# Kernel tuning notes

Hardware: AMD Instinct MI355X
Metric: run time of the kernel (lower is better)

The kernel has to match this reference:

```python
import jax, jax.numpy as jnp
import numpy as np

EMBED_DIM = 1024
Q_HEADS = 8
KV_HEADS = 4
HEAD_DIM = EMBED_DIM // Q_HEADS          # 128
KV_EMBED_DIM = HEAD_DIM * KV_HEADS       # 512
LN_EPS = 1e-5
RMS_EPS = 1e-6


def _activation_quant(x):
    # per-token int8 quant over last dim
    scale = 127.0 / jnp.clip(jnp.max(jnp.abs(x), axis=-1, keepdims=True), 1e-5)
    return jnp.clip(jnp.round(x * scale), -128, 127) / scale


def _weight_quant(w):
    # ternary (sign) quant with global mean-abs scale
    scale = jnp.mean(jnp.abs(w))
    e = jnp.mean(w)
    return jnp.sign(w - e) * scale


def bit_linear(x, w):
    # fresh RMSNorm with weight=ones (as in the torch code: RMSNorm(d)(x))
    x_norm = x * jax.lax.rsqrt(jnp.mean(x * x, axis=-1, keepdims=True) + RMS_EPS)
    # straight-through estimators
    x_q = x_norm + jax.lax.stop_gradient(_activation_quant(x_norm) - x_norm)
    w_q = w + jax.lax.stop_gradient(_weight_quant(w) - w)
    # F.linear(x_quant, w_quant): NO bias (the torch forward ignores self.bias)
    return jnp.einsum('bnd,od->bno', x_q, w_q)


def setup_inputs() -> dict:
    key = jax.random.key(0)
    ks = jax.random.split(key, 7)
    B, S = 4, 2048

    def xavier(k, shape):
        std = (2.0 / (shape[0] + shape[1])) ** 0.5
        return std * jax.random.normal(k, shape, dtype=jnp.float32)

    return {
        'query': jax.random.normal(ks[0], (B, S, EMBED_DIM), dtype=jnp.float32),
        'key':   jax.random.normal(ks[1], (B, S, EMBED_DIM), dtype=jnp.float32),
        'value': jax.random.normal(ks[2], (B, S, EMBED_DIM), dtype=jnp.float32),
        'q_w':   xavier(ks[3], (EMBED_DIM, EMBED_DIM)),
        'k_w':   xavier(ks[4], (KV_EMBED_DIM, EMBED_DIM)),
        'v_w':   xavier(ks[5], (KV_EMBED_DIM, EMBED_DIM)),
        'out_w': xavier(ks[6], (EMBED_DIM, KV_EMBED_DIM)),
        'ln_gamma': jnp.ones((KV_EMBED_DIM,), dtype=jnp.float32),
        'ln_beta':  jnp.zeros((KV_EMBED_DIM,), dtype=jnp.float32),
    }


def reference(query, key, value, q_w, k_w, v_w, out_w, ln_gamma, ln_beta):
    B, N, _ = query.shape
    q = bit_linear(query, q_w)   # [b, n, embed_dim]
    k = bit_linear(key,   k_w)   # [b, s, kv_embed_dim]
    v = bit_linear(value, v_w)   # [b, s, kv_embed_dim]

    g = Q_HEADS // KV_HEADS  # head groups
    # b n (hq d) -> b hq n d -> b hk g n d  (head index = h*g + g_idx, matching
    # einops 'b (h g) n d -> b g h n d')
    q = q.reshape(B, N, Q_HEADS, HEAD_DIM).transpose(0, 2, 1, 3)
    q = q.reshape(B, KV_HEADS, g, N, HEAD_DIM)
    k = k.reshape(B, -1, KV_HEADS, HEAD_DIM).transpose(0, 2, 1, 3)  # b h s d
    v = v.reshape(B, -1, KV_HEADS, HEAD_DIM).transpose(0, 2, 1, 3)  # b h s d

    scale = HEAD_DIM ** 0.5
    q = q / scale
    # note: the original SUMS over the group axis g (faithful to einops einsum)
    sim = jnp.einsum('bhgnd,bhsd->bhns', q, k)
    # note: original divides by scale AGAIN before softmax
    attn = jax.nn.softmax(sim / scale, axis=-1)
    out = jnp.einsum('bhns,bhsd->bnhd', attn, v)        # b n hk d
    x = out.reshape(B, N, KV_EMBED_DIM)

    # LayerNorm over kv_embed_dim
    mu = jnp.mean(x, axis=-1, keepdims=True)
    var = jnp.mean((x - mu) ** 2, axis=-1, keepdims=True)
    x = (x - mu) * jax.lax.rsqrt(var + LN_EPS) * ln_gamma + ln_beta

    return bit_linear(x, out_w)  # [b, n, embed_dim]
```

## Files before the change

kernel.cpp:

```cpp
#include <hip/hip_runtime.h>
#include <cstdint>
#include <cstddef>

constexpr int B_   = 4;
constexpr int SEQ  = 2048;
constexpr int E    = 1024;
constexpr int KVE  = 512;
constexpr int H    = 4;
constexpr int ROWS = B_ * SEQ;

typedef short short8   __attribute__((ext_vector_type(8)));
typedef short short4v  __attribute__((ext_vector_type(4)));
typedef float floatx4  __attribute__((ext_vector_type(4)));
typedef float floatx16 __attribute__((ext_vector_type(16)));
typedef int   intx4    __attribute__((ext_vector_type(4)));

__device__ inline short f2bf(float f) {
    uint32_t u = __builtin_bit_cast(uint32_t, f);
    u = (u + 0x7fff + ((u >> 16) & 1)) >> 16;
    return (short)u;
}
__device__ inline float bf2f(short s) {
    return __builtin_bit_cast(float, (uint32_t)(uint16_t)s << 16);
}
__device__ inline void gl_lds16(const void* g, void* l) {
    __builtin_amdgcn_global_load_lds(
        (const __attribute__((address_space(1))) unsigned int*)g,
        (__attribute__((address_space(3))) unsigned int*)l, 16, 0, 0);
}

__global__ __launch_bounds__(256) void pre_kernel(
    const float* __restrict__ qx, const float* __restrict__ kx,
    const float* __restrict__ vx,
    const float* __restrict__ w0, const float* __restrict__ w1,
    const float* __restrict__ w2, const float* __restrict__ w3,
    int8_t* __restrict__ xq01, int8_t* __restrict__ xq2,
    float* __restrict__ dqv, float* __restrict__ stats)
{
    int tid = threadIdx.x, bid = blockIdx.x;
    int lane = tid & 63, wv = tid >> 6;
    if (bid < 256) {
        int m = bid >> 6;
        const float* w = (m == 0) ? w0 : (m == 1) ? w1 : (m == 2) ? w2 : w3;
        int n4 = ((m == 0) ? 1024 * 1024 : 512 * 1024) >> 2;
        float s = 0.f, sa = 0.f;
        for (int i = (bid & 63) * 256 + tid; i < n4; i += 64 * 256) {
            float4 x = ((const float4*)w)[i];
            s += x.x + x.y + x.z + x.w;
            sa += fabsf(x.x) + fabsf(x.y) + fabsf(x.z) + fabsf(x.w);
        }
#pragma unroll
        for (int o = 32; o; o >>= 1) { s += __shfl_xor(s, o); sa += __shfl_xor(sa, o); }
        __shared__ float ls[4], lsa[4];
        if (!lane) { ls[wv] = s; lsa[wv] = sa; }
        __syncthreads();
        if (!tid) {
            atomicAdd(&stats[2 * m],     ls[0] + ls[1] + ls[2] + ls[3]);
            atomicAdd(&stats[2 * m + 1], lsa[0] + lsa[1] + lsa[2] + lsa[3]);
        }
        return;
    }
    int rowi = (bid - 256) * 4 + wv;
    int z = rowi >> 13, r = rowi & (ROWS - 1);
    const float* x = (z == 0) ? qx : (z == 1) ? kx : vx;
    int8_t* xq = (z == 2) ? xq2 : xq01 + (size_t)z * ROWS * E;
    size_t base = (size_t)r * E;
    float4 v[4];
    float ss = 0.f, am = 0.f;
#pragma unroll
    for (int j = 0; j < 4; j++) {
        v[j] = *(const float4*)(x + base + lane * 4 + j * 256);
        ss += v[j].x * v[j].x + v[j].y * v[j].y + v[j].z * v[j].z + v[j].w * v[j].w;
        am = fmaxf(am, fmaxf(fmaxf(fabsf(v[j].x), fabsf(v[j].y)),
                             fmaxf(fabsf(v[j].z), fabsf(v[j].w))));
    }
#pragma unroll
    for (int o = 32; o; o >>= 1) { ss += __shfl_xor(ss, o); am = fmaxf(am, __shfl_xor(am, o)); }
    float rms = rsqrtf(ss * (1.0f / E) + 1e-6f);
    float cl  = fmaxf(am * rms, 1e-5f);
    float kf  = rms * (127.0f / cl);
#pragma unroll
    for (int j = 0; j < 4; j++) {
        int q0 = max(-128, min(127, (int)rintf(v[j].x * kf)));
        int q1 = max(-128, min(127, (int)rintf(v[j].y * kf)));
        int q2 = max(-128, min(127, (int)rintf(v[j].z * kf)));
        int q3 = max(-128, min(127, (int)rintf(v[j].w * kf)));
        uint32_t pk = (uint32_t)(q0 & 0xff) | ((uint32_t)(q1 & 0xff) << 8) |
                      ((uint32_t)(q2 & 0xff) << 16) | ((uint32_t)(q3 & 0xff) << 24);
        *(uint32_t*)(xq + base + lane * 4 + j * 256) = pk;
    }
    if (!lane) dqv[(size_t)z * ROWS + r] = cl * (1.0f / 127.0f);
}

__global__ __launch_bounds__(256) void wquant_kernel(
    const float* __restrict__ w0, const float* __restrict__ w1,
    const float* __restrict__ w2, const float* __restrict__ w3,
    int n0, int n1, int n2, int n3, const float* __restrict__ stats,
    int8_t* __restrict__ o0, int8_t* __restrict__ o1,
    int8_t* __restrict__ o2, int8_t* __restrict__ o3)
{
    int m = blockIdx.y;
    const float* w = (m == 0) ? w0 : (m == 1) ? w1 : (m == 2) ? w2 : w3;
    int n = (m == 0) ? n0 : (m == 1) ? n1 : (m == 2) ? n2 : n3;
    int8_t* o = (m == 0) ? o0 : (m == 1) ? o1 : (m == 2) ? o2 : o3;
    float e = stats[2 * m] / (float)n;
    int n4 = n >> 2;
    for (int i = blockIdx.x * 256 + threadIdx.x; i < n4; i += gridDim.x * 256) {
        float4 x = ((const float4*)w)[i];
        int q0 = (x.x > e) - (x.x < e);
        int q1 = (x.y > e) - (x.y < e);
        int q2 = (x.z > e) - (x.z < e);
        int q3 = (x.w > e) - (x.w < e);
        uint32_t pk = (uint32_t)(q0 & 0xff) | ((uint32_t)(q1 & 0xff) << 8) |
                      ((uint32_t)(q2 & 0xff) << 16) | ((uint32_t)(q3 & 0xff) << 24);
        *(uint32_t*)(o + ((size_t)i << 2)) = pk;
    }
}

template <bool F32OUT>
__device__ inline void gemm_body(
    const int8_t* __restrict__ A, const int8_t* __restrict__ W,
    const float* __restrict__ dqv, float sw, void* __restrict__ Cout,
    int O, int K, int8_t* As, int8_t* Ws, size_t row0, size_t c0)
{
    int tid = threadIdx.x;
    int w = tid >> 6, lane = tid & 63;
    int quad = lane >> 4, l15 = lane & 15;
    int mbase = (w & 1) * 64, nbase = (w >> 1) * 64;

    intx4 acc[4][4];
#pragma unroll
    for (int i = 0; i < 4; i++)
#pragma unroll
        for (int j = 0; j < 4; j++) acc[i][j] = (intx4){0, 0, 0, 0};

    const int8_t* Ag[4]; const int8_t* Wg[4]; int8_t* lA[4]; int8_t* lW[4];
#pragma unroll
    for (int t = 0; t < 4; t++) {
        int c = tid + t * 256;
        int row = c >> 3, g = (c & 7) ^ (row & 7);
        Ag[t] = A + (row0 + row) * K + g * 16;
        Wg[t] = W + (c0 + row) * K + g * 16;
        lA[t] = As + c * 16;
        lW[t] = Ws + c * 16;
    }

    for (int kt = 0; kt < K; kt += 128) {
        __syncthreads();
#pragma unroll
        for (int t = 0; t < 4; t++) {
            gl_lds16(Ag[t] + kt, lA[t]);
            gl_lds16(Wg[t] + kt, lW[t]);
        }
        __syncthreads();
#pragma unroll
        for (int kh = 0; kh < 2; kh++) {
            intx4 af[4], bfr[4];
#pragma unroll
            for (int mt = 0; mt < 4; mt++) {
                int row = mbase + mt * 16 + l15;
                int pos = (quad + 4 * kh) ^ (row & 7);
                af[mt] = *(const intx4*)(As + row * 128 + pos * 16);
            }
#pragma unroll
            for (int nt = 0; nt < 4; nt++) {
                int row = nbase + nt * 16 + l15;
                int pos = (quad + 4 * kh) ^ (row & 7);
                bfr[nt] = *(const intx4*)(Ws + row * 128 + pos * 16);
            }
#pragma unroll
            for (int mt = 0; mt < 4; mt++)
#pragma unroll
                for (int nt = 0; nt < 4; nt++)
                    acc[mt][nt] = __builtin_amdgcn_mfma_i32_16x16x64_i8(
                        af[mt], bfr[nt], acc[mt][nt], 0, 0, 0);
        }
    }

#pragma unroll
    for (int mt = 0; mt < 4; mt++) {
#pragma unroll
        for (int r = 0; r < 4; r++) {
            size_t grow = row0 + mbase + mt * 16 + quad * 4 + r;
            float scv = sw * dqv[grow];
#pragma unroll
            for (int nt = 0; nt < 4; nt++) {
                size_t gcol = c0 + nbase + nt * 16 + l15;
                float v = (float)acc[mt][nt][r] * scv;
                if constexpr (F32OUT) ((float*)Cout)[grow * O + gcol] = v;
                else                  ((short*)Cout)[grow * O + gcol] = f2bf(v);
            }
        }
    }
}

__global__ __launch_bounds__(256) void gemm_qkv(
    const int8_t* __restrict__ xq01, const int8_t* __restrict__ xq2,
    const int8_t* __restrict__ wq_q, const int8_t* __restrict__ wq_k,
    const int8_t* __restrict__ wq_v, const float* __restrict__ dqv,
    const float* __restrict__ stats,
    short* __restrict__ qb, short* __restrict__ kb, short* __restrict__ vb)
{
    __shared__ int8_t As[128 * 128];
    __shared__ int8_t Ws[128 * 128];
    int id = blockIdx.x;
    int z, bx, by;
    if (id < 512)      { z = 0; bx = id & 7; by = id >> 3; }
    else if (id < 768) { z = 1; int t = id - 512; bx = t & 3; by = t >> 2; }
    else               { z = 2; int t = id - 768; bx = t & 3; by = t >> 2; }
    int O = z ? KVE : E;
    const int8_t* A = (z == 0) ? xq01 : (z == 1) ? xq01 + (size_t)ROWS * E : xq2;
    const int8_t* W = (z == 0) ? wq_q : (z == 1) ? wq_k : wq_v;
    short* outp = (z == 0) ? qb : (z == 1) ? kb : vb;
    float sw = stats[2 * z + 1] / (float)(O * E);
    gemm_body<false>(A, W, dqv + (size_t)z * ROWS, sw, outp, O, E, As, Ws,
                     (size_t)by * 128, (size_t)bx * 128);
}

__global__ __launch_bounds__(256) void gemm_out(
    const int8_t* __restrict__ A, const int8_t* __restrict__ W,
    const float* __restrict__ dqv, const float* __restrict__ stats,
    float* __restrict__ Cout)
{
    __shared__ int8_t As[128 * 128];
    __shared__ int8_t Ws[128 * 128];
    float sw = stats[7] / (float)(E * KVE);
    gemm_body<true>(A, W, dqv, sw, Cout, E, KVE, As, Ws,
                    (size_t)blockIdx.y * 128, (size_t)blockIdx.x * 128);
}

__global__ __launch_bounds__(256, 2) void attn_mfma(
    const short* __restrict__ qb, const short* __restrict__ kb,
    const short* __restrict__ vb, short* __restrict__ opart,
    float* __restrict__ mlbuf)
{
    __shared__ short Ks[64][132];
    __shared__ short Vt[128][68];
    __shared__ short Ps[128][68];
    int tid = threadIdx.x;
    int w = tid >> 6, lane = tid & 63;
    int l31 = lane & 31, hi = lane >> 5;
    int blk = blockIdx.x, h = blockIdx.y, half = blockIdx.z;
    int b = blk >> 4;
    size_t qrow0 = (size_t)blk * 128;
    size_t sbase = (size_t)b * SEQ + (size_t)half * (SEQ / 2);

    int sK = tid >> 2, cK = tid & 3;
    int sV = (tid & 15) * 4, dV = tid >> 4;

    short8 kreg[4], vreg[4];
    {
        const short* ksrc = kb + (sbase + sK) * KVE + h * 128 + cK * 32;
#pragma unroll
        for (int j = 0; j < 4; j++) kreg[j] = *(const short8*)(ksrc + j * 8);
        const short* vsrc = vb + (sbase + sV) * KVE + h * 128 + dV * 8;
#pragma unroll
        for (int j = 0; j < 4; j++) vreg[j] = *(const short8*)(vsrc + j * KVE);
    }

    short8 qfrag[8];
    {
        const short* src = qb + (qrow0 + w * 32 + l31) * E + h * 256 + hi * 8;
#pragma unroll
        for (int j = 0; j < 8; j++) {
            short8 a  = *(const short8*)(src + j * 16);
            short8 b2 = *(const short8*)(src + j * 16 + 128);
            short8 o;
#pragma unroll
            for (int e = 0; e < 8; e++)
                o[e] = f2bf((bf2f(a[e]) + bf2f(b2[e])) * (1.0f / 128.0f));
            qfrag[j] = o;
        }
    }

    floatx16 oacc[4];
#pragma unroll
    for (int dt = 0; dt < 4; dt++)
#pragma unroll
        for (int r = 0; r < 16; r++) oacc[dt][r] = 0.f;
    float m_s = -1e30f, l_s = 0.f;

    for (int st = 0; st < SEQ / 128; st++) {
        __syncthreads();
#pragma unroll
        for (int j = 0; j < 4; j++)
            *(short8*)&Ks[sK][cK * 32 + j * 8] = kreg[j];
#pragma unroll
        for (int i = 0; i < 8; i++) {
            short4v vv = { vreg[0][i], vreg[1][i], vreg[2][i], vreg[3][i] };
            *(short4v*)&Vt[dV * 8 + i][sV] = vv;
        }
        if (st + 1 < SEQ / 128) {
            size_t srow0 = sbase + (size_t)(st + 1) * 64;
            const short* ksrc = kb + (srow0 + sK) * KVE + h * 128 + cK * 32;
#pragma unroll
            for (int j = 0; j < 4; j++) kreg[j] = *(const short8*)(ksrc + j * 8);
            const short* vsrc = vb + (srow0 + sV) * KVE + h * 128 + dV * 8;
#pragma unroll
            for (int j = 0; j < 4; j++) vreg[j] = *(const short8*)(vsrc + j * KVE);
        }
        __syncthreads();
        floatx16 sc0, sc1;
#pragma unroll
        for (int r = 0; r < 16; r++) { sc0[r] = 0.f; sc1[r] = 0.f; }
#pragma unroll
        for (int j = 0; j < 8; j++) {
            short8 kf0 = *(const short8*)&Ks[l31][j * 16 + hi * 8];
            short8 kf1 = *(const short8*)&Ks[32 + l31][j * 16 + hi * 8];
            sc0 = __builtin_amdgcn_mfma_f32_32x32x16_bf16(kf0, qfrag[j], sc0, 0, 0, 0);
            sc1 = __builtin_amdgcn_mfma_f32_32x32x16_bf16(kf1, qfrag[j], sc1, 0, 0, 0);
        }
        float mx = sc0[0];
#pragma unroll
        for (int r = 0; r < 16; r++) { mx = fmaxf(mx, sc0[r]); mx = fmaxf(mx, sc1[r]); }
        mx = fmaxf(mx, __shfl_xor(mx, 32));
        float nm = fmaxf(m_s, mx);
        float alpha = __expf(m_s - nm);
        m_s = nm;
        float rs = 0.f;
#pragma unroll
        for (int r = 0; r < 16; r++) {
            float p0 = __expf(sc0[r] - nm); sc0[r] = p0; rs += p0;
            float p1 = __expf(sc1[r] - nm); sc1[r] = p1; rs += p1;
        }
        rs += __shfl_xor(rs, 32);
        l_s = l_s * alpha + rs;
        int qrow = w * 32 + l31;
#pragma unroll
        for (int c = 0; c < 4; c++) {
            short4v p0 = { f2bf(sc0[c * 4]), f2bf(sc0[c * 4 + 1]),
                           f2bf(sc0[c * 4 + 2]), f2bf(sc0[c * 4 + 3]) };
            *(short4v*)&Ps[qrow][c * 8 + hi * 4] = p0;
            short4v p1 = { f2bf(sc1[c * 4]), f2bf(sc1[c * 4 + 1]),
                           f2bf(sc1[c * 4 + 2]), f2bf(sc1[c * 4 + 3]) };
            *(short4v*)&Ps[qrow][32 + c * 8 + hi * 4] = p1;
        }
#pragma unroll
        for (int dt = 0; dt < 4; dt++)
#pragma unroll
            for (int r = 0; r < 16; r++) oacc[dt][r] *= alpha;
        short8 pb[4];
#pragma unroll
        for (int j = 0; j < 4; j++)
            pb[j] = *(const short8*)&Ps[qrow][j * 16 + hi * 8];
#pragma unroll
        for (int dt = 0; dt < 4; dt++)
#pragma unroll
            for (int j = 0; j < 4; j++) {
                short8 vf = *(const short8*)&Vt[dt * 32 + l31][j * 16 + hi * 8];
                oacc[dt] = __builtin_amdgcn_mfma_f32_32x32x16_bf16(vf, pb[j], oacc[dt], 0, 0, 0);
            }
    }
    {
        float inv = 1.0f / l_s;
        size_t grow = qrow0 + w * 32 + l31;
        short* dst = opart + ((size_t)half * ROWS + grow) * KVE + h * 128;
#pragma unroll
        for (int dt = 0; dt < 4; dt++)
#pragma unroll
            for (int c = 0; c < 4; c++) {
                short4v o4 = { f2bf(oacc[dt][c * 4] * inv),
                               f2bf(oacc[dt][c * 4 + 1] * inv),
                               f2bf(oacc[dt][c * 4 + 2] * inv),
                               f2bf(oacc[dt][c * 4 + 3] * inv) };
                *(short4v*)(dst + dt * 32 + c * 8 + hi * 4) = o4;
            }
        if (hi == 0) {
            float* ml = mlbuf + (((size_t)half * ROWS + grow) * H + h) * 2;
            ml[0] = m_s;
            ml[1] = l_s;
        }
    }
}

__global__ __launch_bounds__(256) void ln_combine_kernel(
    const short* __restrict__ opart, const float* __restrict__ mlbuf,
    const float* __restrict__ gamma, const float* __restrict__ beta,
    int8_t* __restrict__ xq, float* __restrict__ dqv)
{
    int lane = threadIdx.x & 63, wv = threadIdx.x >> 6;
    int row = blockIdx.x * 4 + wv;
    float4 y[2];
    float s = 0.f, ss = 0.f;
#pragma unroll
    for (int j = 0; j < 2; j++) {
        int col = lane * 4 + j * 256;
        int h = j * 2 + (lane >> 5);
        const float* ml0 = mlbuf + ((size_t)row * H + h) * 2;
        const float* ml1 = mlbuf + (((size_t)ROWS + row) * H + h) * 2;
        float m1 = ml0[0], l1v = ml0[1], m2 = ml1[0], l2v = ml1[1];
        float M = fmaxf(m1, m2);
        float w1 = l1v * __expf(m1 - M), w2 = l2v * __expf(m2 - M);
        float winv = 1.0f / (w1 + w2);
        w1 *= winv; w2 *= winv;
        short4v o1 = *(const short4v*)(opart + (size_t)row * KVE + col);
        short4v o2 = *(const short4v*)(opart + ((size_t)ROWS + row) * KVE + col);
        float4 vv = { bf2f(o1.x) * w1 + bf2f(o2.x) * w2,
                      bf2f(o1.y) * w1 + bf2f(o2.y) * w2,
                      bf2f(o1.z) * w1 + bf2f(o2.z) * w2,
                      bf2f(o1.w) * w1 + bf2f(o2.w) * w2 };
        y[j] = vv;
        s += vv.x + vv.y + vv.z + vv.w;
        ss += vv.x * vv.x + vv.y * vv.y + vv.z * vv.z + vv.w * vv.w;
    }
#pragma unroll
    for (int o = 32; o; o >>= 1) { s += __shfl_xor(s, o); ss += __shfl_xor(ss, o); }
    float mu = s * (1.0f / KVE);
    float var = fmaxf(ss * (1.0f / KVE) - mu * mu, 0.0f);
    float inv = rsqrtf(var + 1e-5f);
    float sy = 0.f, am = 0.f;
#pragma unroll
    for (int j = 0; j < 2; j++) {
        int col = lane * 4 + j * 256;
        float4 g = *(const float4*)(gamma + col);
        float4 be = *(const float4*)(beta + col);
        y[j].x = (y[j].x - mu) * inv * g.x + be.x;
        y[j].y = (y[j].y - mu) * inv * g.y + be.y;
        y[j].z = (y[j].z - mu) * inv * g.z + be.z;
        y[j].w = (y[j].w - mu) * inv * g.w + be.w;
        sy += y[j].x * y[j].x + y[j].y * y[j].y + y[j].z * y[j].z + y[j].w * y[j].w;
        am = fmaxf(am, fmaxf(fmaxf(fabsf(y[j].x), fabsf(y[j].y)),
                             fmaxf(fabsf(y[j].z), fabsf(y[j].w))));
    }
#pragma unroll
    for (int o = 32; o; o >>= 1) { sy += __shfl_xor(sy, o); am = fmaxf(am, __shfl_xor(am, o)); }
    float rms = rsqrtf(sy * (1.0f / KVE) + 1e-6f);
    float cl = fmaxf(am * rms, 1e-5f);
    float kf = rms * (127.0f / cl);
#pragma unroll
    for (int j = 0; j < 2; j++) {
        int col = lane * 4 + j * 256;
        int q0 = max(-128, min(127, (int)rintf(y[j].x * kf)));
        int q1 = max(-128, min(127, (int)rintf(y[j].y * kf)));
        int q2 = max(-128, min(127, (int)rintf(y[j].z * kf)));
        int q3 = max(-128, min(127, (int)rintf(y[j].w * kf)));
        uint32_t pk = (uint32_t)(q0 & 0xff) | ((uint32_t)(q1 & 0xff) << 8) |
                      ((uint32_t)(q2 & 0xff) << 16) | ((uint32_t)(q3 & 0xff) << 24);
        *(uint32_t*)(xq + (size_t)row * KVE + col) = pk;
    }
    if (!lane) dqv[row] = cl * (1.0f / 127.0f);
}

extern "C" void kernel_launch(void* const* d_in, const int* in_sizes, int n_in,
                              void* d_out, int out_size, void* d_ws, size_t ws_size,
                              hipStream_t stream)
{
    const float* query = (const float*)d_in[0];
    const float* key   = (const float*)d_in[1];
    const float* value = (const float*)d_in[2];
    const float* q_w   = (const float*)d_in[3];
    const float* k_w   = (const float*)d_in[4];
    const float* v_w   = (const float*)d_in[5];
    const float* out_w = (const float*)d_in[6];
    const float* ln_g  = (const float*)d_in[7];
    const float* ln_b  = (const float*)d_in[8];
    float* out = (float*)d_out;

    char* p = (char*)d_ws;
    float* stats = (float*)p;  p += 256;
    int8_t* wq_q = (int8_t*)p; p += (size_t)1024 * 1024;
    int8_t* wq_k = (int8_t*)p; p += (size_t)512 * 1024;
    int8_t* wq_v = (int8_t*)p; p += (size_t)512 * 1024;
    int8_t* wq_o = (int8_t*)p; p += (size_t)1024 * 512;
    int8_t* xq01 = (int8_t*)p; p += (size_t)2 * ROWS * E;
    float* dqv  = (float*)p;   p += (size_t)3 * ROWS * 4;
    short* qb   = (short*)p;   p += (size_t)ROWS * E * 2;
    short* kb   = (short*)p;   p += (size_t)ROWS * KVE * 2;
    short* vb   = (short*)p;   p += (size_t)ROWS * KVE * 2;
    short* opart = (short*)p;  p += (size_t)2 * ROWS * KVE * 2;
    float* mlbuf = (float*)p;  p += (size_t)2 * ROWS * H * 2 * 4;
    int8_t* xq2 = (int8_t*)opart;
    if ((size_t)(p - (char*)d_ws) > ws_size) return;

    dim3 blk(256);
    hipMemsetAsync(stats, 0, 256, stream);
    pre_kernel<<<dim3(256 + 3 * ROWS / 4), blk, 0, stream>>>(query, key, value,
        q_w, k_w, v_w, out_w, xq01, xq2, dqv, stats);
    wquant_kernel<<<dim3(64, 4), blk, 0, stream>>>(q_w, k_w, v_w, out_w,
        1024 * 1024, 512 * 1024, 512 * 1024, 1024 * 512, stats, wq_q, wq_k, wq_v, wq_o);

    gemm_qkv<<<dim3(1024), blk, 0, stream>>>(xq01, xq2, wq_q, wq_k, wq_v,
        dqv, stats, qb, kb, vb);

    attn_mfma<<<dim3(ROWS / 128, H, 2), blk, 0, stream>>>(qb, kb, vb, opart, mlbuf);

    ln_combine_kernel<<<dim3(ROWS / 4), blk, 0, stream>>>(opart, mlbuf,
        ln_g, ln_b, xq01, dqv);
    gemm_out<<<dim3(8, 64), blk, 0, stream>>>(xq01, wq_o, dqv, stats, out);
}
```

Before: 267.9 us.

## Split attention KV into four parts, precompute scaled Q, keep P in registers

Raises the KV split from two to four, so more attention blocks are launched and each walks a shorter KV range. The LN-combine kernel now merges four partial results. A separate kernel pre-sums the two query groups and folds in the log2(e)/128 scale, which lets the attention loop use exp2 directly. The softmax probabilities are packed with v_cvt_pk_bf16 and rearranged with permlane32_swap instead of a round trip through LDS. Rescaling is skipped unless the running max grows by more than 8. The cost is extra partial-output memory traffic, one more kernel launch, and a lazy-rescale scheme that relies on exp2 values staying bounded.

After: 293.1 us. 9.4% more time.

```diff
diff --git a/kernel.cpp b/kernel.cpp
--- a/kernel.cpp
+++ b/kernel.cpp
@@ -8,6 +8,9 @@
 constexpr int KVE  = 512;
 constexpr int H    = 4;
 constexpr int ROWS = B_ * SEQ;
+constexpr int NSPLIT = 4;
+constexpr int KVT  = SEQ / NSPLIT;
+constexpr int NT   = KVT / 64;
 
 typedef short short8   __attribute__((ext_vector_type(8)));
 typedef short short4v  __attribute__((ext_vector_type(4)));
@@ -229,21 +232,37 @@
                     (size_t)blockIdx.y * 128, (size_t)blockIdx.x * 128);
 }
 
-__global__ __launch_bounds__(256, 2) void attn_mfma(
-    const short* __restrict__ qb, const short* __restrict__ kb,
+__global__ __launch_bounds__(256) void qsum_kernel(
+    const short* __restrict__ qb, short* __restrict__ qs)
+{
+    int lane = threadIdx.x & 63, wv = threadIdx.x >> 6;
+    size_t row = (size_t)blockIdx.x * 4 + wv;
+    int h = lane >> 4, d = (lane & 15) * 8;
+    const short* src = qb + row * E + h * 256 + d;
+    short8 a = *(const short8*)src;
+    short8 b = *(const short8*)(src + 128);
+    short8 o;
+    constexpr float C = 1.44269504089f * (1.0f / 128.0f);
+#pragma unroll
+    for (int e = 0; e < 8; e++)
+        o[e] = f2bf((bf2f(a[e]) + bf2f(b[e])) * C);
+    *(short8*)(qs + row * KVE + (size_t)lane * 8) = o;
+}
+
+__global__ __launch_bounds__(256, 3) void attn_mfma(
+    const short* __restrict__ qs, const short* __restrict__ kb,
     const short* __restrict__ vb, short* __restrict__ opart,
     float* __restrict__ mlbuf)
 {
     __shared__ short Ks[64][132];
     __shared__ short Vt[128][68];
-    __shared__ short Ps[128][68];
     int tid = threadIdx.x;
     int w = tid >> 6, lane = tid & 63;
     int l31 = lane & 31, hi = lane >> 5;
-    int blk = blockIdx.x, h = blockIdx.y, half = blockIdx.z;
+    int blk = blockIdx.x, h = blockIdx.y, part = blockIdx.z;
     int b = blk >> 4;
     size_t qrow0 = (size_t)blk * 128;
-    size_t sbase = (size_t)b * SEQ + (size_t)half * (SEQ / 2);
+    size_t sbase = (size_t)b * SEQ + (size_t)part * KVT;
 
     int sK = tid >> 2, cK = tid & 3;
     int sV = (tid & 15) * 4, dV = tid >> 4;
@@ -260,17 +279,9 @@
 
     short8 qfrag[8];
     {
-        const short* src = qb + (qrow0 + w * 32 + l31) * E + h * 256 + hi * 8;
-#pragma unroll
-        for (int j = 0; j < 8; j++) {
-            short8 a  = *(const short8*)(src + j * 16);
-            short8 b2 = *(const short8*)(src + j * 16 + 128);
-            short8 o;
-#pragma unroll
-            for (int e = 0; e < 8; e++)
-                o[e] = f2bf((bf2f(a[e]) + bf2f(b2[e])) * (1.0f / 128.0f));
-            qfrag[j] = o;
-        }
+        const short* src = qs + (qrow0 + w * 32 + l31) * KVE + h * 128 + hi * 8;
+#pragma unroll
+        for (int j = 0; j < 8; j++) qfrag[j] = *(const short8*)(src + j * 16);
     }
 
     floatx16 oacc[4];
@@ -280,7 +291,7 @@
         for (int r = 0; r < 16; r++) oacc[dt][r] = 0.f;
     float m_s = -1e30f, l_s = 0.f;
 
-    for (int st = 0; st < SEQ / 128; st++) {
+    for (int st = 0; st < NT; st++) {
         __syncthreads();
 #pragma unroll
         for (int j = 0; j < 4; j++)
@@ -290,7 +301,7 @@
             short4v vv = { vreg[0][i], vreg[1][i], vreg[2][i], vreg[3][i] };
             *(short4v*)&Vt[dV * 8 + i][sV] = vv;
         }
-        if (st + 1 < SEQ / 128) {
+        if (st + 1 < NT) {
             size_t srow0 = sbase + (size_t)(st + 1) * 64;
             const short* ksrc = kb + (srow0 + sK) * KVE + h * 128 + cK * 32;
 #pragma unroll
@@ -312,37 +323,56 @@
         }
         float mx = sc0[0];
 #pragma unroll
-        for (int r = 0; r < 16; r++) { mx = fmaxf(mx, sc0[r]); mx = fmaxf(mx, sc1[r]); }
+        for (int r = 0; r < 16; r++) mx = fmaxf(mx, fmaxf(sc0[r], sc1[r]));
         mx = fmaxf(mx, __shfl_xor(mx, 32));
-        float nm = fmaxf(m_s, mx);
-        float alpha = __expf(m_s - nm);
-        m_s = nm;
+        float pm = fmaxf(m_s, mx);
+        if (!__all(pm - m_s <= 8.0f)) {
+            float alpha = __builtin_amdgcn_exp2f(m_s - pm);
+            m_s = pm;
+            l_s *= alpha;
+#pragma unroll
+            for (int dt = 0; dt < 4; dt++)
+#pragma unroll
+                for (int r = 0; r < 16; r++) oacc[dt][r] *= alpha;
+        }
         float rs = 0.f;
 #pragma unroll
         for (int r = 0; r < 16; r++) {
-            float p0 = __expf(sc0[r] - nm); sc0[r] = p0; rs += p0;
-            float p1 = __expf(sc1[r] - nm); sc1[r] = p1; rs += p1;
+            float p0 = __builtin_amdgcn_exp2f(sc0[r] - m_s); sc0[r] = p0; rs += p0;
+            float p1 = __builtin_amdgcn_exp2f(sc1[r] - m_s); sc1[r] = p1; rs += p1;
         }
         rs += __shfl_xor(rs, 32);
-        l_s = l_s * alpha + rs;
-        int qrow = w * 32 + l31;
-#pragma unroll
-        for (int c = 0; c < 4; c++) {
-            short4v p0 = { f2bf(sc0[c * 4]), f2bf(sc0[c * 4 + 1]),
-                           f2bf(sc0[c * 4 + 2]), f2bf(sc0[c * 4 + 3]) };
-            *(short4v*)&Ps[qrow][c * 8 + hi * 4] = p0;
-            short4v p1 = { f2bf(sc1[c * 4]), f2bf(sc1[c * 4 + 1]),
-                           f2bf(sc1[c * 4 + 2]), f2bf(sc1[c * 4 + 3]) };
-            *(short4v*)&Ps[qrow][32 + c * 8 + hi * 4] = p1;
-        }
-#pragma unroll
-        for (int dt = 0; dt < 4; dt++)
-#pragma unroll
-            for (int r = 0; r < 16; r++) oacc[dt][r] *= alpha;
+        l_s += rs;
+        uint32_t w0[8], w1[8];
+#pragma unroll
+        for (int i = 0; i < 8; i++) {
+            asm("v_cvt_pk_bf16_f32 %0, %1, %2"
+                : "=v"(w0[i]) : "v"(sc0[2 * i]), "v"(sc0[2 * i + 1]));
+            asm("v_cvt_pk_bf16_f32 %0, %1, %2"
+                : "=v"(w1[i]) : "v"(sc1[2 * i]), "v"(sc1[2 * i + 1]));
+        }
+#pragma unroll
+        for (int i = 0; i < 2; i++) {
+            { auto r = __builtin_amdgcn_permlane32_swap(w0[i], w0[i + 2], false, false);
+              w0[i] = r[0]; w0[i + 2] = r[1]; }
+            { auto r = __builtin_amdgcn_permlane32_swap(w0[i + 4], w0[i + 6], false, false);
+              w0[i + 4] = r[0]; w0[i + 6] = r[1]; }
+            { auto r = __builtin_amdgcn_permlane32_swap(w1[i], w1[i + 2], false, false);
+              w1[i] = r[0]; w1[i + 2] = r[1]; }
+            { auto r = __builtin_amdgcn_permlane32_swap(w1[i + 4], w1[i + 6], false, false);
+              w1[i + 4] = r[0]; w1[i + 6] = r[1]; }
+        }
         short8 pb[4];
-#pragma unroll
-        for (int j = 0; j < 4; j++)
-            pb[j] = *(const short8*)&Ps[qrow][j * 16 + hi * 8];
+        {
+            intx4 t0 = { (int)w0[0], (int)w0[1], (int)w0[2], (int)w0[3] };
+            intx4 t1 = { (int)w0[4], (int)w0[5], (int)w0[6], (int)w0[7] };
+            intx4 t2 = { (int)w1[0], (int)w1[1], (int)w1[2], (int)w1[3] };
+            intx4 t3 = { (int)w1[4], (int)w1[5], (int)w1[6], (int)w1[7] };
+            pb[0] = __builtin_bit_cast(short8, t0);
+            pb[1] = __builtin_bit_cast(short8, t1);
+            pb[2] = __builtin_bit_cast(short8, t2);
+            pb[3] = __builtin_bit_cast(short8, t3);
+        }
 #pragma unroll
         for (int dt = 0; dt < 4; dt++)
 #pragma unroll
@@ -354,7 +384,7 @@
     {
         float inv = 1.0f / l_s;
         size_t grow = qrow0 + w * 32 + l31;
-        short* dst = opart + ((size_t)half * ROWS + grow) * KVE + h * 128;
+        short* dst = opart + ((size_t)part * ROWS + grow) * KVE + h * 128;
 #pragma unroll
         for (int dt = 0; dt < 4; dt++)
 #pragma unroll
@@ -366,7 +396,7 @@
                 *(short4v*)(dst + dt * 32 + c * 8 + hi * 4) = o4;
             }
         if (hi == 0) {
-            float* ml = mlbuf + (((size_t)half * ROWS + grow) * H + h) * 2;
+            float* ml = mlbuf + (((size_t)part * ROWS + grow) * H + h) * 2;
             ml[0] = m_s;
             ml[1] = l_s;
         }
@@ -386,19 +416,31 @@
     for (int j = 0; j < 2; j++) {
         int col = lane * 4 + j * 256;
         int h = j * 2 + (lane >> 5);
-        const float* ml0 = mlbuf + ((size_t)row * H + h) * 2;
-        const float* ml1 = mlbuf + (((size_t)ROWS + row) * H + h) * 2;
-        float m1 = ml0[0], l1v = ml0[1], m2 = ml1[0], l2v = ml1[1];
-        float M = fmaxf(m1, m2);
-        float w1 = l1v * __expf(m1 - M), w2 = l2v * __expf(m2 - M);
-        float winv = 1.0f / (w1 + w2);
-        w1 *= winv; w2 *= winv;
-        short4v o1 = *(const short4v*)(opart + (size_t)row * KVE + col);
-        short4v o2 = *(const short4v*)(opart + ((size_t)ROWS + row) * KVE + col);
-        float4 vv = { bf2f(o1.x) * w1 + bf2f(o2.x) * w2,
-                      bf2f(o1.y) * w1 + bf2f(o2.y) * w2,
-                      bf2f(o1.z) * w1 + bf2f(o2.z) * w2,
-                      bf2f(o1.w) * w1 + bf2f(o2.w) * w2 };
+        float mv[NSPLIT], lv[NSPLIT];
+        float M = -1e30f;
+#pragma unroll
+        for (int p = 0; p < NSPLIT; p++) {
+            const float* ml = mlbuf + (((size_t)p * ROWS + row) * H + h) * 2;
+            mv[p] = ml[0]; lv[p] = ml[1];
+            M = fmaxf(M, mv[p]);
+        }
+        float wt[NSPLIT], wsum = 0.f;
+#pragma unroll
+        for (int p = 0; p < NSPLIT; p++) {
+            wt[p] = lv[p] * __builtin_amdgcn_exp2f(mv[p] - M);
+            wsum += wt[p];
+        }
+        float winv = 1.0f / wsum;
+        float4 vv = { 0.f, 0.f, 0.f, 0.f };
+#pragma unroll
+        for (int p = 0; p < NSPLIT; p++) {
+            short4v o = *(const short4v*)(opart + ((size_t)p * ROWS + row) * KVE + col);
+            float wp = wt[p] * winv;
+            vv.x += bf2f(o.x) * wp;
+            vv.y += bf2f(o.y) * wp;
+            vv.z += bf2f(o.z) * wp;
+            vv.w += bf2f(o.w) * wp;
+        }
         y[j] = vv;
         s += vv.x + vv.y + vv.z + vv.w;
         ss += vv.x * vv.x + vv.y * vv.y + vv.z * vv.z + vv.w * vv.w;
@@ -467,9 +509,10 @@
     short* qb   = (short*)p;   p += (size_t)ROWS * E * 2;
     short* kb   = (short*)p;   p += (size_t)ROWS * KVE * 2;
     short* vb   = (short*)p;   p += (size_t)ROWS * KVE * 2;
-    short* opart = (short*)p;  p += (size_t)2 * ROWS * KVE * 2;
-    float* mlbuf = (float*)p;  p += (size_t)2 * ROWS * H * 2 * 4;
+    short* opart = (short*)p;  p += (size_t)NSPLIT * ROWS * KVE * 2;
+    float* mlbuf = (float*)p;  p += (size_t)NSPLIT * ROWS * H * 2 * 4;
     int8_t* xq2 = (int8_t*)opart;
+    short* qsum = (short*)xq01;
     if ((size_t)(p - (char*)d_ws) > ws_size) return;
 
     dim3 blk(256);
@@ -482,7 +525,10 @@
     gemm_qkv<<<dim3(1024), blk, 0, stream>>>(xq01, xq2, wq_q, wq_k, wq_v,
         dqv, stats, qb, kb, vb);
 
-    attn_mfma<<<dim3(ROWS / 128, H, 2), blk, 0, stream>>>(qb, kb, vb, opart, mlbuf);
+    qsum_kernel<<<dim3(ROWS / 4), blk, 0, stream>>>(qb, qsum);
+
+    attn_mfma<<<dim3(ROWS / 128, H, NSPLIT), blk, 0, stream>>>(qsum, kb, vb,
+        opart, mlbuf);
 
     ln_combine_kernel<<<dim3(ROWS / 4), blk, 0, stream>>>(opart, mlbuf,
         ln_g, ln_b, xq01, dqv);
```
